# Performance work log

Measured on AMD Instinct MI355X. Metric: run time of the kernel, lower is better.

Reference implementation:

```python
import jax, jax.numpy as jnp
import numpy as np

TAU = 2.0   # membrane time constant
V_TH = 0.5  # firing threshold

@jax.custom_vjp
def spike_fn(v):
    return jnp.where(v > 0, 1.0, 0.0)

def _spike_fwd(v):
    return spike_fn(v), v

def _spike_bwd(v, g):
    # atan surrogate gradient (alpha=2): d s / d v = 1 / (1 + (pi*v)^2)
    sg = 1.0 / (1.0 + (jnp.pi * v) ** 2)
    return (g * sg,)

spike_fn.defvjp(_spike_fwd, _spike_bwd)


def setup_inputs() -> dict:
    key = jax.random.key(0)
    # [batch, neurons, time] -- time on axis 2, matching moveaxis(x, 2, 0)
    x = jax.random.normal(key, (32, 16384, 100), dtype=jnp.float32)
    return {"x": x}


def reference(x):
    x_seq = jnp.moveaxis(x, 2, 0)  # [T, B, N]
    decay = 1.0 - 1.0 / TAU

    def scan_fn(v, x_t):
        v = v * decay + x_t            # leaky integrate
        s = spike_fn(v - V_TH)         # fire
        v = v - s * V_TH               # soft reset
        return v, s

    v_init = jnp.zeros_like(x_seq[0])
    _, spikes = jax.lax.scan(scan_fn, v_init, x_seq)
    return jnp.moveaxis(spikes, 0, 2)  # [B, N, T]
```

## Files before the change

### kernel.cpp

```cpp
#include <hip/hip_runtime.h>


#define T_STEPS 100
#define T_VEC   25
#define ROWS    64
#define HROWS   32
#define SLOTS   26
#define DECAY   0.5f
#define VTH     0.5f

__device__ __forceinline__ int swz(int c4, int row) {
    return (c4 < 24) ? (c4 ^ (row & 7)) : c4;
}

__global__ __launch_bounds__(64, 3) void lif_kernel(const float* __restrict__ x,
                                                    float* __restrict__ out,
                                                    int n_rows) {
    __shared__ float4 tile[HROWS * SLOTS];

    const int tid = threadIdx.x;
    const long long row0 = (long long)blockIdx.x * ROWS;
    const long long my_row = row0 + tid;

    float4 buf[T_VEC];
    if (my_row < n_rows) {
        const float4* __restrict__ xr = reinterpret_cast<const float4*>(x) + my_row * T_VEC;
        float v = 0.0f;
        #pragma unroll
        for (int j = 0; j < T_VEC; ++j) {
            float4 xv = xr[j];
            float xs[4] = {xv.x, xv.y, xv.z, xv.w};
            float ss[4];
            #pragma unroll
            for (int k = 0; k < 4; ++k) {
                v = v * DECAY + xs[k];
                float sk = (v - VTH > 0.0f) ? 1.0f : 0.0f;
                v -= sk * VTH;
                ss[k] = sk;
            }
            buf[j].x = ss[0]; buf[j].y = ss[1]; buf[j].z = ss[2]; buf[j].w = ss[3];
        }
    }

    const long long total_f4 = (long long)n_rows * T_VEC;
    float4* __restrict__ ob = reinterpret_cast<float4*>(out);

    #pragma unroll
    for (int stage = 0; stage < 2; ++stage) {
        const int rbase = stage * HROWS;
        if ((tid >> 5) == stage) {
            const int r = tid & (HROWS - 1);
            #pragma unroll
            for (int j = 0; j < T_VEC; ++j) {
                tile[r * SLOTS + swz(j, r)] = buf[j];
            }
        }
        __syncthreads();

        const long long gbase = (row0 + rbase) * T_VEC;
        #pragma unroll
        for (int k = 0; k < 13; ++k) {
            int f = k * ROWS + tid;
            if (f < HROWS * T_VEC && gbase + f < total_f4) {
                int row = f / T_VEC;
                int c4  = f % T_VEC;
                ob[gbase + f] = tile[row * SLOTS + swz(c4, row)];
            }
        }
        __syncthreads();
    }
}

extern "C" void kernel_launch(void* const* d_in, const int* in_sizes, int n_in,
                              void* d_out, int out_size, void* d_ws, size_t ws_size,
                              hipStream_t stream) {
    const float* x = (const float*)d_in[0];
    float* out = (float*)d_out;

    int n_rows = in_sizes[0] / T_STEPS;
    int grid = (n_rows + ROWS - 1) / ROWS;

    lif_kernel<<<grid, ROWS, 0, stream>>>(x, out, n_rows);
}
```

Baseline: 97.56 us.

## Bit-pack spikes in shared memory and load inputs in chunks

Spike outputs are packed into four 32-bit words per row instead of 25 float4 registers. The packed bits are staged through a much smaller shared tile and expanded back to floats during a single coalesced write pass, which removes the two-stage transpose and one barrier. Inputs are loaded in chunks of five float4 rather than all up front, which lowers register pressure; launch bounds are raised to allow more resident blocks. The cost is extra bit-manipulation ALU work in both the compute and store phases.

```diff
diff --git a/kernel.cpp b/kernel.cpp
--- a/kernel.cpp
+++ b/kernel.cpp
@@ -3,71 +3,78 @@
 
 #define T_STEPS 100
 #define T_VEC   25
+#define CHUNK   5
+#define NCHUNK  5
 #define ROWS    64
-#define HROWS   32
-#define SLOTS   26
 #define DECAY   0.5f
 #define VTH     0.5f
 
-__device__ __forceinline__ int swz(int c4, int row) {
-    return (c4 < 24) ? (c4 ^ (row & 7)) : c4;
-}
+typedef float vfloat4 __attribute__((ext_vector_type(4)));
 
-__global__ __launch_bounds__(64, 3) void lif_kernel(const float* __restrict__ x,
+__global__ __launch_bounds__(64, 6) void lif_kernel(const float* __restrict__ x,
                                                     float* __restrict__ out,
                                                     int n_rows) {
-    __shared__ float4 tile[HROWS * SLOTS];
+    __shared__ unsigned int tile[ROWS * 4];
 
-    const int tid = threadIdx.x;
+    const int lane = threadIdx.x;
     const long long row0 = (long long)blockIdx.x * ROWS;
-    const long long my_row = row0 + tid;
+    const long long my_row = row0 + lane;
 
-    float4 buf[T_VEC];
+    unsigned int pk0 = 0, pk1 = 0, pk2 = 0, pk3 = 0;
+
     if (my_row < n_rows) {
-        const float4* __restrict__ xr = reinterpret_cast<const float4*>(x) + my_row * T_VEC;
+        const vfloat4* __restrict__ xr =
+            reinterpret_cast<const vfloat4*>(x) + my_row * T_VEC;
         float v = 0.0f;
         #pragma unroll
-        for (int j = 0; j < T_VEC; ++j) {
-            float4 xv = xr[j];
-            float xs[4] = {xv.x, xv.y, xv.z, xv.w};
-            float ss[4];
+        for (int c = 0; c < NCHUNK; ++c) {
+            vfloat4 xs[CHUNK];
             #pragma unroll
-            for (int k = 0; k < 4; ++k) {
-                v = v * DECAY + xs[k];
-                float sk = (v - VTH > 0.0f) ? 1.0f : 0.0f;
-                v -= sk * VTH;
-                ss[k] = sk;
+            for (int j = 0; j < CHUNK; ++j) xs[j] = xr[c * CHUNK + j];
+            #pragma unroll
+            for (int j = 0; j < CHUNK; ++j) {
+                #pragma unroll
+                for (int k = 0; k < 4; ++k) {
+                    v = v * DECAY + xs[j][k];
+                    bool sb = (v - VTH > 0.0f);
+                    v -= sb ? VTH : 0.0f;
+                    unsigned int bit = sb ? 1u : 0u;
+                    const int b = c * 20 + j * 4 + k;
+                    if (b < 32)      pk0 |= bit << b;
+                    else if (b < 64) pk1 |= bit << (b - 32);
+                    else if (b < 96) pk2 |= bit << (b - 64);
+                    else             pk3 |= bit << (b - 96);
+                }
             }
-            buf[j].x = ss[0]; buf[j].y = ss[1]; buf[j].z = ss[2]; buf[j].w = ss[3];
         }
     }
 
+    {
+        uint4 w; w.x = pk0; w.y = pk1; w.z = pk2; w.w = pk3;
+        reinterpret_cast<uint4*>(tile)[lane] = w;
+    }
+    __syncthreads();
+
+    vfloat4* __restrict__ ob = reinterpret_cast<vfloat4*>(out);
+    const long long gf0 = row0 * T_VEC;
     const long long total_f4 = (long long)n_rows * T_VEC;
-    float4* __restrict__ ob = reinterpret_cast<float4*>(out);
-
     #pragma unroll
-    for (int stage = 0; stage < 2; ++stage) {
-        const int rbase = stage * HROWS;
-        if ((tid >> 5) == stage) {
-            const int r = tid & (HROWS - 1);
-            #pragma unroll
-            for (int j = 0; j < T_VEC; ++j) {
-                tile[r * SLOTS + swz(j, r)] = buf[j];
-            }
+    for (int i = 0; i < T_VEC; ++i) {
+        int f = i * 64 + lane;
+        long long g = gf0 + f;
+        if (g < total_f4) {
+            int r  = f / T_VEC;
+            int c4 = f % T_VEC;
+            unsigned int word = tile[r * 4 + (c4 >> 3)];
+            int shift = (c4 & 7) * 4;
+            unsigned int nib = (word >> shift) & 0xFu;
+            vfloat4 s;
+            s.x = (nib & 1u) ? 1.0f : 0.0f;
+            s.y = (nib & 2u) ? 1.0f : 0.0f;
+            s.z = (nib & 4u) ? 1.0f : 0.0f;
+            s.w = (nib & 8u) ? 1.0f : 0.0f;
+            ob[g] = s;
         }
-        __syncthreads();
-
-        const long long gbase = (row0 + rbase) * T_VEC;
-        #pragma unroll
-        for (int k = 0; k < 13; ++k) {
-            int f = k * ROWS + tid;
-            if (f < HROWS * T_VEC && gbase + f < total_f4) {
-                int row = f / T_VEC;
-                int c4  = f % T_VEC;
-                ob[gbase + f] = tile[row * SLOTS + swz(c4, row)];
-            }
-        }
-        __syncthreads();
     }
 }
 
```

Result: slower. 118.2 us (+21.2%).
